# Performance work log

Measured on AMD Instinct MI355X. Metric: run time of the kernel, lower is better.

The kernel has to match this reference:

```python
import jax, jax.numpy as jnp
import numpy as np

B, N, D, H = 2048, 64, 256, 16

def setup_inputs() -> dict:
    key = jax.random.key(0)
    ks = jax.random.split(key, 6)
    members_embeds = jax.random.normal(ks[0], (B, N, D), dtype=jnp.float32)
    item_embeds = jax.random.normal(ks[1], (B, D), dtype=jnp.float32)
    # MLP params: Linear(D,16) -> ReLU -> Linear(16,1)
    W1 = jax.random.normal(ks[2], (D, H), dtype=jnp.float32) * (1.0 / np.sqrt(D))
    b1 = jnp.zeros((H,), dtype=jnp.float32)
    W2 = jax.random.normal(ks[3], (H, 1), dtype=jnp.float32) * (1.0 / np.sqrt(H))
    b2 = jnp.zeros((1,), dtype=jnp.float32)
    return {"members_embeds": members_embeds, "item_embeds": item_embeds,
            "W1": W1, "b1": b1, "W2": W2, "b2": b2}

def reference(members_embeds, item_embeds, W1, b1, W2, b2):
    # Original: diff_i = sum_{j != i} (u_i - u_j) * item  ==  (N*u_i - sum_j u_j) * item
    n = members_embeds.shape[1]
    total = jnp.sum(members_embeds, axis=1, keepdims=True)           # [B,1,D]
    diff = (n * members_embeds - total) * item_embeds[:, None, :]    # [B,N,D]
    h = jax.nn.relu(jnp.einsum('bnd,dh->bnh', diff, W1) + b1)        # [B,N,16]
    logits = (jnp.einsum('bnh,ho->bno', h, W2) + b2)[..., 0]         # [B,N]
    return jax.nn.softmax(logits, axis=1)                            # weights over members
```

## Files before the change

kernel.cpp:

```cpp
#include <hip/hip_runtime.h>


static constexpr int NMEM  = 64;
static constexpr int DDIM  = 256;
static constexpr int TD    = 32;
static constexpr int NTILE = DDIM / TD;
static constexpr int UTS   = 36;
static constexpr int UTS4  = UTS / 4;

__device__ __forceinline__ void fma4(float4& acc, float s, const float4& w) {
    acc.x = fmaf(s, w.x, acc.x);
    acc.y = fmaf(s, w.y, acc.y);
    acc.z = fmaf(s, w.z, acc.z);
    acc.w = fmaf(s, w.w, acc.w);
}

__global__ __launch_bounds__(256, 2)
void attn_group_softmax(const float* __restrict__ u_g,
                        const float* __restrict__ item_g,
                        const float* __restrict__ W1,
                        const float* __restrict__ b1,
                        const float* __restrict__ W2,
                        float* __restrict__ out)
{
    __shared__ float w1s[DDIM * 16];
    __shared__ float item_s[4][DDIM];
    __shared__ float ut[4][NMEM * UTS];

    const int tid  = threadIdx.x;
    const int w    = tid >> 6;
    const int lane = tid & 63;
    const int b    = blockIdx.x * 4 + w;

    {
        const float4* src = (const float4*)W1;
        float4* dst = (float4*)w1s;
        #pragma unroll
        for (int i = 0; i < 4; ++i) dst[tid + 256 * i] = src[tid + 256 * i];
    }
    {
        const float4* src = (const float4*)(item_g + (size_t)b * DDIM);
        ((float4*)item_s[w])[lane] = src[lane];
    }
    __syncthreads();

    const int q    = lane & 3;
    const int n0   = lane >> 2;
    const int col4 = lane & 7;
    const int row0 = lane >> 3;

    const float4* ug4  = (const float4*)u_g + (size_t)b * (NMEM * DDIM / 4);
    const float4* it4p = (const float4*)item_s[w];
    float4*       uts4 = (float4*)ut[w];
    const float4* utf4 = (const float4*)ut[w];
    const float4* w1s4 = (const float4*)w1s;

    float4 acc0 = make_float4(0.f, 0.f, 0.f, 0.f);
    float4 acc1 = acc0, acc2 = acc0, acc3 = acc0;

    float4 r[8];
    #pragma unroll
    for (int i = 0; i < 8; ++i)
        r[i] = ug4[(row0 + 8 * i) * (DDIM / 4) + col4];

    for (int t = 0; t < NTILE; ++t) {
        const float4 itv = it4p[t * 8 + col4];
        #pragma unroll
        for (int i = 0; i < 8; ++i) {
            float4 v = r[i];
            v.x *= itv.x; v.y *= itv.y; v.z *= itv.z; v.w *= itv.w;
            uts4[(row0 + 8 * i) * UTS4 + col4] = v;
        }
        __syncthreads();

        if (t + 1 < NTILE) {
            #pragma unroll
            for (int i = 0; i < 8; ++i)
                r[i] = ug4[(row0 + 8 * i) * (DDIM / 4) + (t + 1) * 8 + col4];
        }

        #pragma unroll
        for (int d4 = 0; d4 < TD / 4; ++d4) {
            const float4 ua = utf4[(n0     ) * UTS4 + d4];
            const float4 ub = utf4[(n0 + 16) * UTS4 + d4];
            const float4 uc = utf4[(n0 + 32) * UTS4 + d4];
            const float4 ud = utf4[(n0 + 48) * UTS4 + d4];
            const int dbase = (t * TD + d4 * 4) * 4 + q;
            const float4 w0  = w1s4[dbase];
            const float4 w1r = w1s4[dbase + 4];
            const float4 w2r = w1s4[dbase + 8];
            const float4 w3r = w1s4[dbase + 12];
            fma4(acc0, ua.x, w0); fma4(acc0, ua.y, w1r); fma4(acc0, ua.z, w2r); fma4(acc0, ua.w, w3r);
            fma4(acc1, ub.x, w0); fma4(acc1, ub.y, w1r); fma4(acc1, ub.z, w2r); fma4(acc1, ub.w, w3r);
            fma4(acc2, uc.x, w0); fma4(acc2, uc.y, w1r); fma4(acc2, uc.z, w2r); fma4(acc2, uc.w, w3r);
            fma4(acc3, ud.x, w0); fma4(acc3, ud.y, w1r); fma4(acc3, ud.z, w2r); fma4(acc3, ud.w, w3r);
        }
        __syncthreads();
    }

    float4 tt;
    tt.x = acc0.x + acc1.x + acc2.x + acc3.x;
    tt.y = acc0.y + acc1.y + acc2.y + acc3.y;
    tt.z = acc0.z + acc1.z + acc2.z + acc3.z;
    tt.w = acc0.w + acc1.w + acc2.w + acc3.w;
    #pragma unroll
    for (int off = 4; off <= 32; off <<= 1) {
        tt.x += __shfl_xor(tt.x, off, 64);
        tt.y += __shfl_xor(tt.y, off, 64);
        tt.z += __shfl_xor(tt.z, off, 64);
        tt.w += __shfl_xor(tt.w, off, 64);
    }

    const float4 b1v = ((const float4*)b1)[q];
    const float4 w2v = ((const float4*)W2)[q];

    auto logit_part = [&](const float4& a) -> float {
        const float zx = fmaxf(fmaf(64.f, a.x, b1v.x - tt.x), 0.f);
        const float zy = fmaxf(fmaf(64.f, a.y, b1v.y - tt.y), 0.f);
        const float zz = fmaxf(fmaf(64.f, a.z, b1v.z - tt.z), 0.f);
        const float zw = fmaxf(fmaf(64.f, a.w, b1v.w - tt.w), 0.f);
        return zx * w2v.x + zy * w2v.y + zz * w2v.z + zw * w2v.w;
    };

    float p0 = logit_part(acc0);
    float p1 = logit_part(acc1);
    float p2 = logit_part(acc2);
    float p3 = logit_part(acc3);
    p0 += __shfl_xor(p0, 1, 64); p0 += __shfl_xor(p0, 2, 64);
    p1 += __shfl_xor(p1, 1, 64); p1 += __shfl_xor(p1, 2, 64);
    p2 += __shfl_xor(p2, 1, 64); p2 += __shfl_xor(p2, 2, 64);
    p3 += __shfl_xor(p3, 1, 64); p3 += __shfl_xor(p3, 2, 64);

    float m = fmaxf(fmaxf(p0, p1), fmaxf(p2, p3));
    #pragma unroll
    for (int off = 4; off <= 32; off <<= 1) m = fmaxf(m, __shfl_xor(m, off, 64));
    const float e0 = __expf(p0 - m);
    const float e1 = __expf(p1 - m);
    const float e2 = __expf(p2 - m);
    const float e3 = __expf(p3 - m);
    float s = e0 + e1 + e2 + e3;
    #pragma unroll
    for (int off = 4; off <= 32; off <<= 1) s += __shfl_xor(s, off, 64);
    const float inv = 1.0f / s;

    if (q == 0) {
        float* ob = out + (size_t)b * NMEM + n0;
        ob[0]  = e0 * inv;
        ob[16] = e1 * inv;
        ob[32] = e2 * inv;
        ob[48] = e3 * inv;
    }
}

extern "C" void kernel_launch(void* const* d_in, const int* in_sizes, int n_in,
                              void* d_out, int out_size, void* d_ws, size_t ws_size,
                              hipStream_t stream) {
    const float* u    = (const float*)d_in[0];
    const float* item = (const float*)d_in[1];
    const float* W1   = (const float*)d_in[2];
    const float* b1   = (const float*)d_in[3];
    const float* W2   = (const float*)d_in[4];
    (void)in_sizes; (void)n_in; (void)out_size; (void)d_ws; (void)ws_size;

    attn_group_softmax<<<512, 256, 0, stream>>>(u, item, W1, b1, W2, (float*)d_out);
}
```

Before: 205.3 us.

## Drop per-tile block barriers, swizzle LDS tile, keep item vector in registers

Each wavefront only touches its own shared-memory tile, so the two __syncthreads per tile are removed and ordering relies on the lockstep execution of a single 64-lane wave. The padded tile stride is replaced by an XOR swizzle on float4 columns to avoid bank conflicts without extra LDS. The item vector is preloaded into registers instead of staged through shared memory. This saves barrier stalls and LDS space, but adds register pressure and depends on wave-synchronous LDS ordering for correctness.

```diff
diff --git a/kernel.cpp b/kernel.cpp
--- a/kernel.cpp
+++ b/kernel.cpp
@@ -5,8 +5,7 @@
 static constexpr int DDIM  = 256;
 static constexpr int TD    = 32;
 static constexpr int NTILE = DDIM / TD;
-static constexpr int UTS   = 36;
-static constexpr int UTS4  = UTS / 4;
+static constexpr int UTS4  = TD / 4;
 
 __device__ __forceinline__ void fma4(float4& acc, float s, const float4& w) {
     acc.x = fmaf(s, w.x, acc.x);
@@ -24,8 +23,7 @@
                         float* __restrict__ out)
 {
     __shared__ float w1s[DDIM * 16];
-    __shared__ float item_s[4][DDIM];
-    __shared__ float ut[4][NMEM * UTS];
+    __shared__ float ut[4][NMEM * TD];
 
     const int tid  = threadIdx.x;
     const int w    = tid >> 6;
@@ -38,22 +36,24 @@
         #pragma unroll
         for (int i = 0; i < 4; ++i) dst[tid + 256 * i] = src[tid + 256 * i];
     }
-    {
-        const float4* src = (const float4*)(item_g + (size_t)b * DDIM);
-        ((float4*)item_s[w])[lane] = src[lane];
-    }
     __syncthreads();
 
     const int q    = lane & 3;
     const int n0   = lane >> 2;
     const int col4 = lane & 7;
     const int row0 = lane >> 3;
+    const int sc   = col4 ^ row0;
+    const int pk   = n0 & 7;
 
     const float4* ug4  = (const float4*)u_g + (size_t)b * (NMEM * DDIM / 4);
-    const float4* it4p = (const float4*)item_s[w];
+    const float4* ig4  = (const float4*)(item_g + (size_t)b * DDIM);
     float4*       uts4 = (float4*)ut[w];
     const float4* utf4 = (const float4*)ut[w];
     const float4* w1s4 = (const float4*)w1s;
+
+    float4 itv[NTILE];
+    #pragma unroll
+    for (int t = 0; t < NTILE; ++t) itv[t] = ig4[t * 8 + col4];
 
     float4 acc0 = make_float4(0.f, 0.f, 0.f, 0.f);
     float4 acc1 = acc0, acc2 = acc0, acc3 = acc0;
@@ -64,15 +64,13 @@
         r[i] = ug4[(row0 + 8 * i) * (DDIM / 4) + col4];
 
     for (int t = 0; t < NTILE; ++t) {
-        const float4 itv = it4p[t * 8 + col4];
+        const float4 iv = itv[t];
         #pragma unroll
         for (int i = 0; i < 8; ++i) {
             float4 v = r[i];
-            v.x *= itv.x; v.y *= itv.y; v.z *= itv.z; v.w *= itv.w;
-            uts4[(row0 + 8 * i) * UTS4 + col4] = v;
+            v.x *= iv.x; v.y *= iv.y; v.z *= iv.z; v.w *= iv.w;
+            uts4[(row0 + 8 * i) * UTS4 + sc] = v;
         }
-        __syncthreads();
-
         if (t + 1 < NTILE) {
             #pragma unroll
             for (int i = 0; i < 8; ++i)
@@ -81,10 +79,11 @@
 
         #pragma unroll
         for (int d4 = 0; d4 < TD / 4; ++d4) {
-            const float4 ua = utf4[(n0     ) * UTS4 + d4];
-            const float4 ub = utf4[(n0 + 16) * UTS4 + d4];
-            const float4 uc = utf4[(n0 + 32) * UTS4 + d4];
-            const float4 ud = utf4[(n0 + 48) * UTS4 + d4];
+            const int p = d4 ^ pk;
+            const float4 ua = utf4[(n0     ) * UTS4 + p];
+            const float4 ub = utf4[(n0 + 16) * UTS4 + p];
+            const float4 uc = utf4[(n0 + 32) * UTS4 + p];
+            const float4 ud = utf4[(n0 + 48) * UTS4 + p];
             const int dbase = (t * TD + d4 * 4) * 4 + q;
             const float4 w0  = w1s4[dbase];
             const float4 w1r = w1s4[dbase + 4];
@@ -95,7 +94,6 @@
             fma4(acc2, uc.x, w0); fma4(acc2, uc.y, w1r); fma4(acc2, uc.z, w2r); fma4(acc2, uc.w, w3r);
             fma4(acc3, ud.x, w0); fma4(acc3, ud.y, w1r); fma4(acc3, ud.z, w2r); fma4(acc3, ud.w, w3r);
         }
-        __syncthreads();
     }
 
     float4 tt;
```

Measured after the change: 209.3 us. No clear change (+1.9%).

## Split each batch row across two waves and drop per-tile block barriers

Applied to the files above, without the earlier changes.

Each batch element's 64 members are now split across two wavefronts of 32 members each, so each block handles 2 batch elements and the grid doubles. Per-thread registers and per-wave LDS tiles shrink, and the launch bound rises to 4 blocks per CU to raise occupancy and hide global-load latency. The two halves combine the column sum, softmax max and softmax sum through small shared arrays with extra block barriers. The per-tile __syncthreads are removed, relying on each wave owning a private LDS tile. The trade-off is W1 being copied into LDS by twice as many blocks.

```diff
diff --git a/kernel.cpp b/kernel.cpp
--- a/kernel.cpp
+++ b/kernel.cpp
@@ -15,7 +15,7 @@
     acc.w = fmaf(s, w.w, acc.w);
 }
 
-__global__ __launch_bounds__(256, 2)
+__global__ __launch_bounds__(256, 4)
 void attn_group_softmax(const float* __restrict__ u_g,
                         const float* __restrict__ item_g,
                         const float* __restrict__ W1,
@@ -23,14 +23,18 @@
                         const float* __restrict__ W2,
                         float* __restrict__ out)
 {
-    __shared__ float w1s[DDIM * 16];
-    __shared__ float item_s[4][DDIM];
-    __shared__ float ut[4][NMEM * UTS];
+    __shared__ float  w1s[DDIM * 16];
+    __shared__ float  item_s[2][DDIM];
+    __shared__ float  ut[4][32 * UTS];
+    __shared__ float4 xtt[2][2][4];
+    __shared__ float  xm[2][2], xs[2][2];
 
     const int tid  = threadIdx.x;
     const int w    = tid >> 6;
     const int lane = tid & 63;
-    const int b    = blockIdx.x * 4 + w;
+    const int bb   = w >> 1;
+    const int wh   = w & 1;
+    const int b    = blockIdx.x * 2 + bb;
 
     {
         const float4* src = (const float4*)W1;
@@ -38,10 +42,9 @@
         #pragma unroll
         for (int i = 0; i < 4; ++i) dst[tid + 256 * i] = src[tid + 256 * i];
     }
-    {
-        const float4* src = (const float4*)(item_g + (size_t)b * DDIM);
-        ((float4*)item_s[w])[lane] = src[lane];
-    }
+    if (wh == 0)
+        ((float4*)item_s[bb])[lane] =
+            ((const float4*)(item_g + (size_t)b * DDIM))[lane];
     __syncthreads();
 
     const int q    = lane & 3;
@@ -49,66 +52,67 @@
     const int col4 = lane & 7;
     const int row0 = lane >> 3;
 
-    const float4* ug4  = (const float4*)u_g + (size_t)b * (NMEM * DDIM / 4);
-    const float4* it4p = (const float4*)item_s[w];
+    const float4* ug4  = (const float4*)u_g + (size_t)b * (NMEM * DDIM / 4)
+                       + (32 * wh) * (DDIM / 4);
+    const float4* it4p = (const float4*)item_s[bb];
     float4*       uts4 = (float4*)ut[w];
     const float4* utf4 = (const float4*)ut[w];
     const float4* w1s4 = (const float4*)w1s;
 
     float4 acc0 = make_float4(0.f, 0.f, 0.f, 0.f);
-    float4 acc1 = acc0, acc2 = acc0, acc3 = acc0;
+    float4 acc1 = acc0;
 
-    float4 r[8];
+    float4 r[4];
     #pragma unroll
-    for (int i = 0; i < 8; ++i)
+    for (int i = 0; i < 4; ++i)
         r[i] = ug4[(row0 + 8 * i) * (DDIM / 4) + col4];
 
     for (int t = 0; t < NTILE; ++t) {
         const float4 itv = it4p[t * 8 + col4];
         #pragma unroll
-        for (int i = 0; i < 8; ++i) {
+        for (int i = 0; i < 4; ++i) {
             float4 v = r[i];
             v.x *= itv.x; v.y *= itv.y; v.z *= itv.z; v.w *= itv.w;
             uts4[(row0 + 8 * i) * UTS4 + col4] = v;
         }
-        __syncthreads();
-
         if (t + 1 < NTILE) {
             #pragma unroll
-            for (int i = 0; i < 8; ++i)
+            for (int i = 0; i < 4; ++i)
                 r[i] = ug4[(row0 + 8 * i) * (DDIM / 4) + (t + 1) * 8 + col4];
         }
-
         #pragma unroll
         for (int d4 = 0; d4 < TD / 4; ++d4) {
             const float4 ua = utf4[(n0     ) * UTS4 + d4];
             const float4 ub = utf4[(n0 + 16) * UTS4 + d4];
-            const float4 uc = utf4[(n0 + 32) * UTS4 + d4];
-            const float4 ud = utf4[(n0 + 48) * UTS4 + d4];
             const int dbase = (t * TD + d4 * 4) * 4 + q;
             const float4 w0  = w1s4[dbase];
             const float4 w1r = w1s4[dbase + 4];
             const float4 w2r = w1s4[dbase + 8];
             const float4 w3r = w1s4[dbase + 12];
-            fma4(acc0, ua.x, w0); fma4(acc0, ua.y, w1r); fma4(acc0, ua.z, w2r); fma4(acc0, ua.w, w3r);
-            fma4(acc1, ub.x, w0); fma4(acc1, ub.y, w1r); fma4(acc1, ub.z, w2r); fma4(acc1, ub.w, w3r);
-            fma4(acc2, uc.x, w0); fma4(acc2, uc.y, w1r); fma4(acc2, uc.z, w2r); fma4(acc2, uc.w, w3r);
-            fma4(acc3, ud.x, w0); fma4(acc3, ud.y, w1r); fma4(acc3, ud.z, w2r); fma4(acc3, ud.w, w3r);
+            fma4(acc0, ua.x, w0); fma4(acc0, ua.y, w1r);
+            fma4(acc0, ua.z, w2r); fma4(acc0, ua.w, w3r);
+            fma4(acc1, ub.x, w0); fma4(acc1, ub.y, w1r);
+            fma4(acc1, ub.z, w2r); fma4(acc1, ub.w, w3r);
         }
-        __syncthreads();
     }
 
     float4 tt;
-    tt.x = acc0.x + acc1.x + acc2.x + acc3.x;
-    tt.y = acc0.y + acc1.y + acc2.y + acc3.y;
-    tt.z = acc0.z + acc1.z + acc2.z + acc3.z;
-    tt.w = acc0.w + acc1.w + acc2.w + acc3.w;
+    tt.x = acc0.x + acc1.x;
+    tt.y = acc0.y + acc1.y;
+    tt.z = acc0.z + acc1.z;
+    tt.w = acc0.w + acc1.w;
     #pragma unroll
     for (int off = 4; off <= 32; off <<= 1) {
         tt.x += __shfl_xor(tt.x, off, 64);
         tt.y += __shfl_xor(tt.y, off, 64);
         tt.z += __shfl_xor(tt.z, off, 64);
         tt.w += __shfl_xor(tt.w, off, 64);
+    }
+    if (lane < 4) xtt[bb][wh][lane] = tt;
+    __syncthreads();
+    {
+        const float4 o = xtt[bb][wh ^ 1][q];
+        tt.x += o.x; tt.y += o.y; tt.z += o.z; tt.w += o.w;
     }
 
     const float4 b1v = ((const float4*)b1)[q];
@@ -124,31 +128,29 @@
 
     float p0 = logit_part(acc0);
     float p1 = logit_part(acc1);
-    float p2 = logit_part(acc2);
-    float p3 = logit_part(acc3);
     p0 += __shfl_xor(p0, 1, 64); p0 += __shfl_xor(p0, 2, 64);
     p1 += __shfl_xor(p1, 1, 64); p1 += __shfl_xor(p1, 2, 64);
-    p2 += __shfl_xor(p2, 1, 64); p2 += __shfl_xor(p2, 2, 64);
-    p3 += __shfl_xor(p3, 1, 64); p3 += __shfl_xor(p3, 2, 64);
 
-    float m = fmaxf(fmaxf(p0, p1), fmaxf(p2, p3));
+    float mw = fmaxf(p0, p1);
     #pragma unroll
-    for (int off = 4; off <= 32; off <<= 1) m = fmaxf(m, __shfl_xor(m, off, 64));
+    for (int off = 4; off <= 32; off <<= 1) mw = fmaxf(mw, __shfl_xor(mw, off, 64));
+    if (lane == 0) xm[bb][wh] = mw;
+    __syncthreads();
+    const float m = fmaxf(mw, xm[bb][wh ^ 1]);
+
     const float e0 = __expf(p0 - m);
     const float e1 = __expf(p1 - m);
-    const float e2 = __expf(p2 - m);
-    const float e3 = __expf(p3 - m);
-    float s = e0 + e1 + e2 + e3;
+    float sw = e0 + e1;
     #pragma unroll
-    for (int off = 4; off <= 32; off <<= 1) s += __shfl_xor(s, off, 64);
-    const float inv = 1.0f / s;
+    for (int off = 4; off <= 32; off <<= 1) sw += __shfl_xor(sw, off, 64);
+    if (lane == 0) xs[bb][wh] = sw;
+    __syncthreads();
+    const float inv = 1.0f / (sw + xs[bb][wh ^ 1]);
 
     if (q == 0) {
-        float* ob = out + (size_t)b * NMEM + n0;
+        float* ob = out + (size_t)b * NMEM + 32 * wh + n0;
         ob[0]  = e0 * inv;
         ob[16] = e1 * inv;
-        ob[32] = e2 * inv;
-        ob[48] = e3 * inv;
     }
 }
 
@@ -162,5 +164,5 @@
     const float* W2   = (const float*)d_in[4];
     (void)in_sizes; (void)n_in; (void)out_size; (void)d_ws; (void)ws_size;
 
-    attn_group_softmax<<<512, 256, 0, stream>>>(u, item, W1, b1, W2, (float*)d_out);
+    attn_group_softmax<<<1024, 256, 0, stream>>>(u, item, W1, b1, W2, (float*)d_out);
 }
```

After: 203.0 us. About the same (-1.2%).
